# Performance work log

Measured on AMD Instinct MI355X. Metric: run time of the kernel, lower is better.

## Reference

```python
import jax, jax.numpy as jnp
import numpy as np

MODEL_DIM = 1024
HEADS = 16
HEAD_DIM = MODEL_DIM // HEADS
SEQ = 1024


def setup_inputs() -> dict:
    key0 = jax.random.key(0)
    ks = jax.random.split(key0, 10)
    D, H, d, S = MODEL_DIM, HEADS, HEAD_DIM, SEQ
    s = 1.0 / np.sqrt(D)
    return {
        "value": jax.random.normal(ks[0], (S, D), dtype=jnp.float32),
        "key": jax.random.normal(ks[1], (S, D), dtype=jnp.float32),
        "query": jax.random.normal(ks[2], (S, D), dtype=jnp.float32),
        # per-head projection weights, torch Linear layout (out=d, in=D), stacked over heads
        "Wq": jax.random.uniform(ks[3], (H, d, D), jnp.float32, -s, s),
        "Wk": jax.random.uniform(ks[4], (H, d, D), jnp.float32, -s, s),
        "Wv": jax.random.uniform(ks[5], (H, d, D), jnp.float32, -s, s),
        # u, v biases: torch.rand -> uniform [0,1)
        "u": jax.random.uniform(ks[6], (H, d), dtype=jnp.float32),
        "v": jax.random.uniform(ks[7], (H, d), dtype=jnp.float32),
        "Wo": jax.random.uniform(ks[8], (D, D), jnp.float32, -s, s),
        "bo": jax.random.uniform(ks[9], (D,), jnp.float32, -s, s),
    }


def _rel_pos_R(d, Sq, Sk):
    # pos[i, j] = i - j (Transformer-XL style relative offsets)
    pos = (jnp.arange(Sq)[:, None] - jnp.arange(Sk)[None, :]).astype(jnp.float32)
    inv_freq = 10000.0 ** (-2.0 * jnp.arange(d // 2, dtype=jnp.float32) / d)  # (d/2,)
    ang = pos[None, :, :] * inv_freq[:, None, None]  # (d/2, Sq, Sk)
    # interleave: R[2i] = sin(ang_i), R[2i+1] = cos(ang_i)
    R = jnp.stack([jnp.sin(ang), jnp.cos(ang)], axis=1).reshape(d, Sq, Sk)
    return R


def reference(value, key, query, Wq, Wk, Wv, u, v, Wo, bo):
    # defaults of original forward: scale=True, mask=False
    H, d, D = Wq.shape
    Sq, Sk = query.shape[0], key.shape[0]
    q = jnp.einsum("hdD,sD->hsd", Wq, query)   # (H, Sq, d)
    k = jnp.einsum("hdD,tD->htd", Wk, key)     # (H, Sk, d)
    vals = jnp.einsum("hdD,tD->htd", Wv, value)  # (H, Sk, d)

    R = _rel_pos_R(d, Sq, Sk)  # (d, Sq, Sk)

    cc = jnp.einsum("hsd,htd->hst", q, k)       # content-content
    cp = jnp.einsum("hsd,dst->hst", q, R)       # content-position
    uk = jnp.einsum("hd,htd->ht", u, k)[:, None, :]  # global content bias
    vr = jnp.einsum("hd,dst->hst", v, R)        # global position bias

    att = (cc + cp + uk + vr) * (d ** -0.5)
    att = jax.nn.softmax(att, axis=2)

    out = jnp.einsum("hst,htd->hsd", att, vals)  # (H, Sq, d)
    out = out.transpose(1, 0, 2).reshape(Sq, H * d)  # concat heads along feature dim
    return out @ Wo.T + bo
```

## Files before the change

kernel.cpp:

```cpp
#include <hip/hip_runtime.h>
#include <math.h>

#define SQ 1024
#define DIM 1024
#define NH 16
#define HDIM 64

typedef short bf16x8 __attribute__((ext_vector_type(8)));
typedef float f32x4 __attribute__((ext_vector_type(4)));

__device__ __forceinline__ unsigned short f2bf(float x) {
  unsigned int u = __builtin_bit_cast(unsigned int, x);
  u += 0x7FFFu + ((u >> 16) & 1u);
  return (unsigned short)(u >> 16);
}
__device__ __forceinline__ unsigned int pkbf(float a, float b) {
  return (unsigned)f2bf(a) | ((unsigned)f2bf(b) << 16);
}

__global__ __launch_bounds__(256) void prep_kernel(
    const float* __restrict__ query, const float* __restrict__ key_,
    const float* __restrict__ value, const float* __restrict__ Wq,
    const float* __restrict__ Wk, const float* __restrict__ Wv,
    const float* __restrict__ Wo, unsigned short* __restrict__ bfin,
    unsigned short* __restrict__ Rc)
{
  const int b = blockIdx.x;
  if (b < 3584) {
    int gid = b * 256 + threadIdx.x;
    int seg = gid >> 17;
    int off = (gid & 131071) * 8;
    const float* s = seg == 0 ? query : seg == 1 ? key_ : seg == 2 ? value :
                     seg == 3 ? Wq : seg == 4 ? Wk : seg == 5 ? Wv : Wo;
    float4 a = *(const float4*)&s[off];
    float4 c = *(const float4*)&s[off + 4];
    uint4 o;
    o.x = pkbf(a.x, a.y); o.y = pkbf(a.z, a.w);
    o.z = pkbf(c.x, c.y); o.w = pkbf(c.z, c.w);
    *(uint4*)&bfin[(size_t)gid * 8] = o;
  } else {
    int gid = (b - 3584) * 256 + threadIdx.x;
    int p = gid >> 5, f = gid & 31;
    float pos = (float)(p - (SQ - 1));
    float invf = expf(-0.28782313662425575f * (float)f);
    float ang = pos * invf;
    Rc[p * HDIM + 2 * f]     = f2bf(sinf(ang));
    Rc[p * HDIM + 2 * f + 1] = f2bf(cosf(ang));
  }
}

__global__ __launch_bounds__(256) void gemm_qkv(
    const unsigned short* __restrict__ bfin,
    unsigned short* __restrict__ qu, unsigned short* __restrict__ qv,
    unsigned short* __restrict__ kkp, unsigned short* __restrict__ vvpT,
    const float* __restrict__ u, const float* __restrict__ v)
{
  __shared__ short As[2][64 * 72];
  __shared__ short Bs[2][64 * 72];
  const int z = blockIdx.z;
  const unsigned short* A = bfin + (size_t)z * (1 << 20);
  const unsigned short* B = bfin + (size_t)(3 + z) * (1 << 20);
  const int tid = threadIdx.x;
  const int bm = blockIdx.y * 64, bn = blockIdx.x * 64;
  const int w = tid >> 6, l = tid & 63, g = l >> 4, q = l & 15;
  const int wr = w >> 1, wc = w & 1;
  const int srow = tid >> 2, sc = (tid & 3) * 16;
  const unsigned short* Arow = A + (bm + srow) * DIM + sc;
  const unsigned short* Brow = B + (bn + srow) * DIM + sc;
  f32x4 acc[2][2] = {};

  uint4 a0 = *(const uint4*)&Arow[0];
  uint4 a1 = *(const uint4*)&Arow[8];
  uint4 b0 = *(const uint4*)&Brow[0];
  uint4 b1 = *(const uint4*)&Brow[8];
  *(uint4*)&As[0][srow * 72 + sc]     = a0;
  *(uint4*)&As[0][srow * 72 + sc + 8] = a1;
  *(uint4*)&Bs[0][srow * 72 + sc]     = b0;
  *(uint4*)&Bs[0][srow * 72 + sc + 8] = b1;
  __syncthreads();

  #pragma unroll 2
  for (int k0 = 0; k0 < DIM; k0 += 64) {
    const int cur = (k0 >> 6) & 1;
    const bool more = (k0 + 64 < DIM);
    if (more) {
      a0 = *(const uint4*)&Arow[k0 + 64];
      a1 = *(const uint4*)&Arow[k0 + 64 + 8];
      b0 = *(const uint4*)&Brow[k0 + 64];
      b1 = *(const uint4*)&Brow[k0 + 64 + 8];
    }
    #pragma unroll
    for (int ks = 0; ks < 2; ks++) {
      bf16x8 fa0 = *(const bf16x8*)&As[cur][(wr * 32 + q) * 72      + ks * 32 + g * 8];
      bf16x8 fa1 = *(const bf16x8*)&As[cur][(wr * 32 + 16 + q) * 72 + ks * 32 + g * 8];
      bf16x8 fb0 = *(const bf16x8*)&Bs[cur][(wc * 32 + q) * 72      + ks * 32 + g * 8];
      bf16x8 fb1 = *(const bf16x8*)&Bs[cur][(wc * 32 + 16 + q) * 72 + ks * 32 + g * 8];
      acc[0][0] = __builtin_amdgcn_mfma_f32_16x16x32_bf16(fa0, fb0, acc[0][0], 0, 0, 0);
      acc[0][1] = __builtin_amdgcn_mfma_f32_16x16x32_bf16(fa0, fb1, acc[0][1], 0, 0, 0);
      acc[1][0] = __builtin_amdgcn_mfma_f32_16x16x32_bf16(fa1, fb0, acc[1][0], 0, 0, 0);
      acc[1][1] = __builtin_amdgcn_mfma_f32_16x16x32_bf16(fa1, fb1, acc[1][1], 0, 0, 0);
    }
    if (more) {
      *(uint4*)&As[cur ^ 1][srow * 72 + sc]     = a0;
      *(uint4*)&As[cur ^ 1][srow * 72 + sc + 8] = a1;
      *(uint4*)&Bs[cur ^ 1][srow * 72 + sc]     = b0;
      *(uint4*)&Bs[cur ^ 1][srow * 72 + sc + 8] = b1;
      __syncthreads();
    }
  }

  #pragma unroll
  for (int i = 0; i < 2; i++) {
    #pragma unroll
    for (int j = 0; j < 2; j++) {
      const int m0 = bm + wr * 32 + i * 16 + g * 4;
      const int n  = bn + wc * 32 + j * 16 + q;
      if (z == 0) {
        float uu = u[n], vv = v[n];
        #pragma unroll
        for (int r = 0; r < 4; r++) {
          qu[(m0 + r) * DIM + n] = f2bf((acc[i][j][r] + uu) * 0.125f);
          qv[(m0 + r) * DIM + n] = f2bf((acc[i][j][r] + vv) * 0.125f);
        }
      } else if (z == 1) {
        #pragma unroll
        for (int r = 0; r < 4; r++)
          kkp[(m0 + r) * DIM + n] = f2bf(acc[i][j][r]);
      } else {
        ushort4 pk;
        pk.x = f2bf(acc[i][j][0]); pk.y = f2bf(acc[i][j][1]);
        pk.z = f2bf(acc[i][j][2]); pk.w = f2bf(acc[i][j][3]);
        *(ushort4*)&vvpT[n * SQ + m0] = pk;
      }
    }
  }
}

__global__ __launch_bounds__(256) void gemm_out(
    const unsigned short* __restrict__ A, const unsigned short* __restrict__ B,
    float* __restrict__ out, const float* __restrict__ bo)
{
  __shared__ short As[2][64 * 72];
  __shared__ short Bs[2][64 * 72];
  const int tid = threadIdx.x;
  const int bm = blockIdx.y * 64, bn = blockIdx.x * 64;
  const int w = tid >> 6, l = tid & 63, g = l >> 4, q = l & 15;
  const int wr = w >> 1, wc = w & 1;
  const int srow = tid >> 2, sc = (tid & 3) * 16;
  const unsigned short* Arow = A + (bm + srow) * DIM + sc;
  const unsigned short* Brow = B + (bn + srow) * DIM + sc;
  f32x4 acc[2][2] = {};

  uint4 a0 = *(const uint4*)&Arow[0];
  uint4 a1 = *(const uint4*)&Arow[8];
  uint4 b0 = *(const uint4*)&Brow[0];
  uint4 b1 = *(const uint4*)&Brow[8];
  *(uint4*)&As[0][srow * 72 + sc]     = a0;
  *(uint4*)&As[0][srow * 72 + sc + 8] = a1;
  *(uint4*)&Bs[0][srow * 72 + sc]     = b0;
  *(uint4*)&Bs[0][srow * 72 + sc + 8] = b1;
  __syncthreads();

  #pragma unroll 2
  for (int k0 = 0; k0 < DIM; k0 += 64) {
    const int cur = (k0 >> 6) & 1;
    const bool more = (k0 + 64 < DIM);
    if (more) {
      a0 = *(const uint4*)&Arow[k0 + 64];
      a1 = *(const uint4*)&Arow[k0 + 64 + 8];
      b0 = *(const uint4*)&Brow[k0 + 64];
      b1 = *(const uint4*)&Brow[k0 + 64 + 8];
    }
    #pragma unroll
    for (int ks = 0; ks < 2; ks++) {
      bf16x8 fa0 = *(const bf16x8*)&As[cur][(wr * 32 + q) * 72      + ks * 32 + g * 8];
      bf16x8 fa1 = *(const bf16x8*)&As[cur][(wr * 32 + 16 + q) * 72 + ks * 32 + g * 8];
      bf16x8 fb0 = *(const bf16x8*)&Bs[cur][(wc * 32 + q) * 72      + ks * 32 + g * 8];
      bf16x8 fb1 = *(const bf16x8*)&Bs[cur][(wc * 32 + 16 + q) * 72 + ks * 32 + g * 8];
      acc[0][0] = __builtin_amdgcn_mfma_f32_16x16x32_bf16(fa0, fb0, acc[0][0], 0, 0, 0);
      acc[0][1] = __builtin_amdgcn_mfma_f32_16x16x32_bf16(fa0, fb1, acc[0][1], 0, 0, 0);
      acc[1][0] = __builtin_amdgcn_mfma_f32_16x16x32_bf16(fa1, fb0, acc[1][0], 0, 0, 0);
      acc[1][1] = __builtin_amdgcn_mfma_f32_16x16x32_bf16(fa1, fb1, acc[1][1], 0, 0, 0);
    }
    if (more) {
      *(uint4*)&As[cur ^ 1][srow * 72 + sc]     = a0;
      *(uint4*)&As[cur ^ 1][srow * 72 + sc + 8] = a1;
      *(uint4*)&Bs[cur ^ 1][srow * 72 + sc]     = b0;
      *(uint4*)&Bs[cur ^ 1][srow * 72 + sc + 8] = b1;
      __syncthreads();
    }
  }

  #pragma unroll
  for (int i = 0; i < 2; i++) {
    #pragma unroll
    for (int j = 0; j < 2; j++) {
      const int m0 = bm + wr * 32 + i * 16 + g * 4;
      const int n  = bn + wc * 32 + j * 16 + q;
      float bb = bo[n];
      #pragma unroll
      for (int r = 0; r < 4; r++)
        out[(m0 + r) * DIM + n] = acc[i][j][r] + bb;
    }
  }
}

__global__ __launch_bounds__(256) void attn_mfma(
    const unsigned short* __restrict__ qu, const unsigned short* __restrict__ qv,
    const unsigned short* __restrict__ kkp, const unsigned short* __restrict__ vvpT,
    const unsigned short* __restrict__ Rc, float* __restrict__ PO,
    float* __restrict__ ML)
{
  __shared__ short Ks[64 * 72];
  __shared__ short Vs[64 * 72];
  __shared__ short Rcs[128 * 72];
  __shared__ short Ps[64 * 72];
  __shared__ float Gs[64 * 84];

  const int tid = threadIdx.x;
  const int h  = blockIdx.x >> 4;
  const int s0 = (blockIdx.x & 15) * 64;
  const int th = blockIdx.y;
  const int w = tid >> 6, l = tid & 63, g = l >> 4, q = l & 15;
  const int col0 = h * HDIM;

  const int sw = s0 + w * 16 + q;
  bf16x8 qub[2], qvb[2];
  qub[0] = *(const bf16x8*)&qu[sw * DIM + col0 + g * 8];
  qub[1] = *(const bf16x8*)&qu[sw * DIM + col0 + 32 + g * 8];
  qvb[0] = *(const bf16x8*)&qv[sw * DIM + col0 + g * 8];
  qvb[1] = *(const bf16x8*)&qv[sw * DIM + col0 + 32 + g * 8];

  f32x4 accO[4] = {};
  float m_run = -1e30f, l_run = 0.f;

  const int srow = tid >> 2, sc = (tid & 3) * 16;
  const int rrow = tid >> 1, rc = (tid & 1) * 32;

  const int tstart = th * 512, tend = th * 512 + 512;

  uint4 kr0, kr1, vr0, vr1, rr0, rr1, rr2, rr3;
  {
    const int t0 = tstart;
    kr0 = *(const uint4*)&kkp[(t0 + srow) * DIM + col0 + sc];
    kr1 = *(const uint4*)&kkp[(t0 + srow) * DIM + col0 + sc + 8];
    vr0 = *(const uint4*)&vvpT[(col0 + srow) * SQ + t0 + sc];
    vr1 = *(const uint4*)&vvpT[(col0 + srow) * SQ + t0 + sc + 8];
    const int P0 = s0 - t0 + 960;
    rr0 = *(const uint4*)&Rc[(P0 + rrow) * HDIM + rc];
    rr1 = *(const uint4*)&Rc[(P0 + rrow) * HDIM + rc + 8];
    rr2 = *(const uint4*)&Rc[(P0 + rrow) * HDIM + rc + 16];
    rr3 = *(const uint4*)&Rc[(P0 + rrow) * HDIM + rc + 24];
    *(uint4*)&Ks[srow * 72 + sc]      = kr0;
    *(uint4*)&Ks[srow * 72 + sc + 8]  = kr1;
    *(uint4*)&Vs[srow * 72 + sc]      = vr0;
    *(uint4*)&Vs[srow * 72 + sc + 8]  = vr1;
    *(uint4*)&Rcs[rrow * 72 + rc]      = rr0;
    *(uint4*)&Rcs[rrow * 72 + rc + 8]  = rr1;
    *(uint4*)&Rcs[rrow * 72 + rc + 16] = rr2;
    *(uint4*)&Rcs[rrow * 72 + rc + 24] = rr3;
  }
  __syncthreads();

  for (int t0 = tstart; t0 < tend; t0 += 64) {
    const bool more = (t0 + 64 < tend);
    if (more) {
      const int tn = t0 + 64;
      kr0 = *(const uint4*)&kkp[(tn + srow) * DIM + col0 + sc];
      kr1 = *(const uint4*)&kkp[(tn + srow) * DIM + col0 + sc + 8];
      vr0 = *(const uint4*)&vvpT[(col0 + srow) * SQ + tn + sc];
      vr1 = *(const uint4*)&vvpT[(col0 + srow) * SQ + tn + sc + 8];
      const int P0 = s0 - tn + 960;
      rr0 = *(const uint4*)&Rc[(P0 + rrow) * HDIM + rc];
      rr1 = *(const uint4*)&Rc[(P0 + rrow) * HDIM + rc + 8];
      rr2 = *(const uint4*)&Rc[(P0 + rrow) * HDIM + rc + 16];
      rr3 = *(const uint4*)&Rc[(P0 + rrow) * HDIM + rc + 24];
    }

    f32x4 accS[4] = {};
    f32x4 accG[5] = {};
    #pragma unroll
    for (int ks = 0; ks < 2; ks++) {
      #pragma unroll
      for (int tf = 0; tf < 4; tf++) {
        bf16x8 a = *(const bf16x8*)&Ks[(tf * 16 + q) * 72 + ks * 32 + g * 8];
        accS[tf] = __builtin_amdgcn_mfma_f32_16x16x32_bf16(a, qub[ks], accS[tf], 0, 0, 0);
      }
      #pragma unroll
      for (int pf = 0; pf < 5; pf++) {
        bf16x8 a = *(const bf16x8*)&Rcs[(w * 16 + pf * 16 + q) * 72 + ks * 32 + g * 8];
        accG[pf] = __builtin_amdgcn_mfma_f32_16x16x32_bf16(a, qvb[ks], accG[pf], 0, 0, 0);
      }
    }
    #pragma unroll
    for (int pf = 0; pf < 5; pf++)
      *(f32x4*)&Gs[(w * 16 + q) * 84 + pf * 16 + g * 4] = accG[pf];

    float pvals[16];
    float mx = -1e30f;
    #pragma unroll
    for (int tf = 0; tf < 4; tf++) {
      #pragma unroll
      for (int r = 0; r < 4; r++) {
        int t_rel = tf * 16 + g * 4 + r;
        float sval = accS[tf][r] + Gs[(w * 16 + q) * 84 + (q - t_rel + 63)];
        pvals[tf * 4 + r] = sval;
        mx = fmaxf(mx, sval);
      }
    }
    mx = fmaxf(mx, __shfl_xor(mx, 16));
    mx = fmaxf(mx, __shfl_xor(mx, 32));
    float m_new = fmaxf(m_run, mx);
    float scale = __expf(m_run - m_new);
    float rsum = 0.f;
    #pragma unroll
    for (int i = 0; i < 16; i++) {
      float p = __expf(pvals[i] - m_new);
      pvals[i] = p;
      rsum += p;
    }
    rsum += __shfl_xor(rsum, 16);
    rsum += __shfl_xor(rsum, 32);
    l_run = l_run * scale + rsum;
    m_run = m_new;
    #pragma unroll
    for (int df = 0; df < 4; df++) {
      #pragma unroll
      for (int r = 0; r < 4; r++) accO[df][r] *= scale;
    }
    #pragma unroll
    for (int tf = 0; tf < 4; tf++) {
      unsigned int lo = pkbf(pvals[tf * 4 + 0], pvals[tf * 4 + 1]);
      unsigned int hi = pkbf(pvals[tf * 4 + 2], pvals[tf * 4 + 3]);
      *(uint2*)&Ps[(w * 16 + q) * 72 + tf * 16 + g * 4] = make_uint2(lo, hi);
    }
    #pragma unroll
    for (int ks = 0; ks < 2; ks++) {
      bf16x8 b = *(const bf16x8*)&Ps[(w * 16 + q) * 72 + ks * 32 + g * 8];
      #pragma unroll
      for (int df = 0; df < 4; df++) {
        bf16x8 a = *(const bf16x8*)&Vs[(df * 16 + q) * 72 + ks * 32 + g * 8];
        accO[df] = __builtin_amdgcn_mfma_f32_16x16x32_bf16(a, b, accO[df], 0, 0, 0);
      }
    }

    if (more) {
      __syncthreads();
      *(uint4*)&Ks[srow * 72 + sc]      = kr0;
      *(uint4*)&Ks[srow * 72 + sc + 8]  = kr1;
      *(uint4*)&Vs[srow * 72 + sc]      = vr0;
      *(uint4*)&Vs[srow * 72 + sc + 8]  = vr1;
      *(uint4*)&Rcs[rrow * 72 + rc]      = rr0;
      *(uint4*)&Rcs[rrow * 72 + rc + 8]  = rr1;
      *(uint4*)&Rcs[rrow * 72 + rc + 16] = rr2;
      *(uint4*)&Rcs[rrow * 72 + rc + 24] = rr3;
      __syncthreads();
    }
  }

  const int tile = blockIdx.x * 2 + th;
  float* POt = PO + (size_t)tile * 4096;
  const int sl = w * 16 + q;
  #pragma unroll
  for (int df = 0; df < 4; df++)
    *(f32x4*)&POt[sl * 64 + df * 16 + g * 4] = accO[df];
  if (g == 0) {
    ML[tile * 128 + sl * 2]     = m_run;
    ML[tile * 128 + sl * 2 + 1] = l_run;
  }
}

__global__ __launch_bounds__(256) void attn_combine(
    const float* __restrict__ PO, const float* __restrict__ ML,
    unsigned short* __restrict__ attout)
{
  int gid = blockIdx.x * 256 + threadIdx.x;
  int s  = gid >> 8;
  int c  = (gid & 255) * 4;
  int h  = c >> 6;
  int sb = s >> 6, sl = s & 63;
  int tA = (h * 16 + sb) * 2, tB = tA + 1;
  float mA = ML[tA * 128 + sl * 2], lA = ML[tA * 128 + sl * 2 + 1];
  float mB = ML[tB * 128 + sl * 2], lB = ML[tB * 128 + sl * 2 + 1];
  float m = fmaxf(mA, mB);
  float wA = __expf(mA - m), wB = __expf(mB - m);
  float inv = 1.f / (lA * wA + lB * wB);
  wA *= inv; wB *= inv;
  int dl = c & 63;
  float4 a = *(const float4*)&PO[(size_t)tA * 4096 + sl * 64 + dl];
  float4 b = *(const float4*)&PO[(size_t)tB * 4096 + sl * 64 + dl];
  uint2 o;
  o.x = pkbf(a.x * wA + b.x * wB, a.y * wA + b.y * wB);
  o.y = pkbf(a.z * wA + b.z * wB, a.w * wA + b.w * wB);
  *(uint2*)&attout[s * DIM + c] = o;
}

extern "C" void kernel_launch(void* const* d_in, const int* in_sizes, int n_in,
                              void* d_out, int out_size, void* d_ws, size_t ws_size,
                              hipStream_t stream) {
  const float* value = (const float*)d_in[0];
  const float* key   = (const float*)d_in[1];
  const float* query = (const float*)d_in[2];
  const float* Wq    = (const float*)d_in[3];
  const float* Wk    = (const float*)d_in[4];
  const float* Wv    = (const float*)d_in[5];
  const float* u     = (const float*)d_in[6];
  const float* v     = (const float*)d_in[7];
  const float* Wo    = (const float*)d_in[8];
  const float* bo    = (const float*)d_in[9];
  float* out = (float*)d_out;

  unsigned short* ws = (unsigned short*)d_ws;
  unsigned short* bfin   = ws;
  unsigned short* qu_p   = bfin   + 7 * (1 << 20);
  unsigned short* qv_p   = qu_p   + (1 << 20);
  unsigned short* kkp    = qv_p   + (1 << 20);
  unsigned short* vvpT   = kkp    + (1 << 20);
  unsigned short* attout = vvpT   + (1 << 20);
  unsigned short* Rc     = attout + (1 << 20);
  float* PO = (float*)(Rc + 2048 * 64);
  float* ML = PO + (size_t)512 * 4096;

  prep_kernel<<<3840, 256, 0, stream>>>(query, key, value, Wq, Wk, Wv, Wo, bfin, Rc);

  dim3 gqkv(16, 16, 3);
  gemm_qkv<<<gqkv, 256, 0, stream>>>(bfin, qu_p, qv_p, kkp, vvpT, u, v);

  dim3 gattn(NH * (SQ / 64), 2);
  attn_mfma<<<gattn, 256, 0, stream>>>(qu_p, qv_p, kkp, vvpT, Rc, PO, ML);
  attn_combine<<<1024, 256, 0, stream>>>(PO, ML, attout);

  dim3 gg(16, 16);
  gemm_out<<<gg, 256, 0, stream>>>(attout, bfin + 6 * (1 << 20), out, bo);
}
```

Measured before the change: 142.0 us.

## Fuse split-K attention halves into one block and shrink output GEMM tiles

The attention kernel now runs both key halves as two 4-wave groups inside a single 512-thread block and merges their partial outputs through shared memory. This removes the separate combine kernel, one launch, and the global PO/ML round trip. The relative-position tile is no longer staged in shared memory; its MFMA fragments are read directly from global memory, trading LDS staging and barriers for uncached-pattern global loads. The output GEMM uses 32x64 tiles, doubling the block count to improve occupancy, at the cost of half the threads idling on A-tile loads.

```diff
diff --git a/kernel.cpp b/kernel.cpp
--- a/kernel.cpp
+++ b/kernel.cpp
@@ -140,25 +140,30 @@
     const unsigned short* __restrict__ A, const unsigned short* __restrict__ B,
     float* __restrict__ out, const float* __restrict__ bo)
 {
-  __shared__ short As[2][64 * 72];
+  __shared__ short As[2][32 * 72];
   __shared__ short Bs[2][64 * 72];
   const int tid = threadIdx.x;
-  const int bm = blockIdx.y * 64, bn = blockIdx.x * 64;
+  const int bm = blockIdx.y * 32, bn = blockIdx.x * 64;
   const int w = tid >> 6, l = tid & 63, g = l >> 4, q = l & 15;
   const int wr = w >> 1, wc = w & 1;
-  const int srow = tid >> 2, sc = (tid & 3) * 16;
-  const unsigned short* Arow = A + (bm + srow) * DIM + sc;
-  const unsigned short* Brow = B + (bn + srow) * DIM + sc;
-  f32x4 acc[2][2] = {};
-
-  uint4 a0 = *(const uint4*)&Arow[0];
-  uint4 a1 = *(const uint4*)&Arow[8];
-  uint4 b0 = *(const uint4*)&Brow[0];
-  uint4 b1 = *(const uint4*)&Brow[8];
-  *(uint4*)&As[0][srow * 72 + sc]     = a0;
-  *(uint4*)&As[0][srow * 72 + sc + 8] = a1;
-  *(uint4*)&Bs[0][srow * 72 + sc]     = b0;
-  *(uint4*)&Bs[0][srow * 72 + sc + 8] = b1;
+  const int srowB = tid >> 2, scB = (tid & 3) * 16;
+  const int srowA = (tid & 127) >> 2, scA = (tid & 3) * 16;
+  const bool doA = (tid < 128);
+  const unsigned short* ArowP = A + (bm + srowA) * DIM + scA;
+  const unsigned short* BrowP = B + (bn + srowB) * DIM + scB;
+  f32x4 acc[2] = {};
+
+  uint4 a0 = {}, a1 = {};
+  uint4 b0 = *(const uint4*)&BrowP[0];
+  uint4 b1 = *(const uint4*)&BrowP[8];
+  if (doA) {
+    a0 = *(const uint4*)&ArowP[0];
+    a1 = *(const uint4*)&ArowP[8];
+    *(uint4*)&As[0][srowA * 72 + scA]     = a0;
+    *(uint4*)&As[0][srowA * 72 + scA + 8] = a1;
+  }
+  *(uint4*)&Bs[0][srowB * 72 + scB]     = b0;
+  *(uint4*)&Bs[0][srowB * 72 + scB + 8] = b1;
   __syncthreads();
 
   #pragma unroll 2
@@ -166,65 +171,63 @@
     const int cur = (k0 >> 6) & 1;
     const bool more = (k0 + 64 < DIM);
     if (more) {
-      a0 = *(const uint4*)&Arow[k0 + 64];
-      a1 = *(const uint4*)&Arow[k0 + 64 + 8];
-      b0 = *(const uint4*)&Brow[k0 + 64];
-      b1 = *(const uint4*)&Brow[k0 + 64 + 8];
+      if (doA) {
+        a0 = *(const uint4*)&ArowP[k0 + 64];
+        a1 = *(const uint4*)&ArowP[k0 + 64 + 8];
+      }
+      b0 = *(const uint4*)&BrowP[k0 + 64];
+      b1 = *(const uint4*)&BrowP[k0 + 64 + 8];
     }
     #pragma unroll
     for (int ks = 0; ks < 2; ks++) {
-      bf16x8 fa0 = *(const bf16x8*)&As[cur][(wr * 32 + q) * 72      + ks * 32 + g * 8];
-      bf16x8 fa1 = *(const bf16x8*)&As[cur][(wr * 32 + 16 + q) * 72 + ks * 32 + g * 8];
+      bf16x8 fa  = *(const bf16x8*)&As[cur][(wr * 16 + q) * 72      + ks * 32 + g * 8];
       bf16x8 fb0 = *(const bf16x8*)&Bs[cur][(wc * 32 + q) * 72      + ks * 32 + g * 8];
       bf16x8 fb1 = *(const bf16x8*)&Bs[cur][(wc * 32 + 16 + q) * 72 + ks * 32 + g * 8];
-      acc[0][0] = __builtin_amdgcn_mfma_f32_16x16x32_bf16(fa0, fb0, acc[0][0], 0, 0, 0);
-      acc[0][1] = __builtin_amdgcn_mfma_f32_16x16x32_bf16(fa0, fb1, acc[0][1], 0, 0, 0);
-      acc[1][0] = __builtin_amdgcn_mfma_f32_16x16x32_bf16(fa1, fb0, acc[1][0], 0, 0, 0);
-      acc[1][1] = __builtin_amdgcn_mfma_f32_16x16x32_bf16(fa1, fb1, acc[1][1], 0, 0, 0);
-    }
-    if (more) {
-      *(uint4*)&As[cur ^ 1][srow * 72 + sc]     = a0;
-      *(uint4*)&As[cur ^ 1][srow * 72 + sc + 8] = a1;
-      *(uint4*)&Bs[cur ^ 1][srow * 72 + sc]     = b0;
-      *(uint4*)&Bs[cur ^ 1][srow * 72 + sc + 8] = b1;
+      acc[0] = __builtin_amdgcn_mfma_f32_16x16x32_bf16(fa, fb0, acc[0], 0, 0, 0);
+      acc[1] = __builtin_amdgcn_mfma_f32_16x16x32_bf16(fa, fb1, acc[1], 0, 0, 0);
+    }
+    if (more) {
       __syncthreads();
+      if (doA) {
+        *(uint4*)&As[cur ^ 1][srowA * 72 + scA]     = a0;
+        *(uint4*)&As[cur ^ 1][srowA * 72 + scA + 8] = a1;
+      }
+      *(uint4*)&Bs[cur ^ 1][srowB * 72 + scB]     = b0;
+      *(uint4*)&Bs[cur ^ 1][srowB * 72 + scB + 8] = b1;
+      __syncthreads();
     }
   }
 
   #pragma unroll
-  for (int i = 0; i < 2; i++) {
-    #pragma unroll
-    for (int j = 0; j < 2; j++) {
-      const int m0 = bm + wr * 32 + i * 16 + g * 4;
-      const int n  = bn + wc * 32 + j * 16 + q;
-      float bb = bo[n];
-      #pragma unroll
-      for (int r = 0; r < 4; r++)
-        out[(m0 + r) * DIM + n] = acc[i][j][r] + bb;
-    }
-  }
-}
-
-__global__ __launch_bounds__(256) void attn_mfma(
+  for (int j = 0; j < 2; j++) {
+    const int m0 = bm + wr * 16 + g * 4;
+    const int n  = bn + wc * 32 + j * 16 + q;
+    float bb = bo[n];
+    #pragma unroll
+    for (int r = 0; r < 4; r++)
+      out[(m0 + r) * DIM + n] = acc[j][r] + bb;
+  }
+}
+
+__global__ __launch_bounds__(512) void attn_mfma(
     const unsigned short* __restrict__ qu, const unsigned short* __restrict__ qv,
     const unsigned short* __restrict__ kkp, const unsigned short* __restrict__ vvpT,
-    const unsigned short* __restrict__ Rc, float* __restrict__ PO,
-    float* __restrict__ ML)
+    const unsigned short* __restrict__ Rc, unsigned short* __restrict__ attout)
 {
-  __shared__ short Ks[64 * 72];
-  __shared__ short Vs[64 * 72];
-  __shared__ short Rcs[128 * 72];
-  __shared__ short Ps[64 * 72];
-  __shared__ float Gs[64 * 84];
+  __shared__ short Ks[2][64 * 72];
+  __shared__ short Vs[2][64 * 72];
+  __shared__ short Ps[2][64 * 72];
+  __shared__ float Gs[2][64 * 84];
+  __shared__ float2 mlS[2][64];
 
   const int tid = threadIdx.x;
   const int h  = blockIdx.x >> 4;
   const int s0 = (blockIdx.x & 15) * 64;
-  const int th = blockIdx.y;
-  const int w = tid >> 6, l = tid & 63, g = l >> 4, q = l & 15;
+  const int w = tid >> 6, th = w >> 2, ws = w & 3;
+  const int l = tid & 63, g = l >> 4, q = l & 15;
   const int col0 = h * HDIM;
 
-  const int sw = s0 + w * 16 + q;
+  const int sw = s0 + ws * 16 + q;
   bf16x8 qub[2], qvb[2];
   qub[0] = *(const bf16x8*)&qu[sw * DIM + col0 + g * 8];
   qub[1] = *(const bf16x8*)&qu[sw * DIM + col0 + 32 + g * 8];
@@ -234,31 +237,20 @@
   f32x4 accO[4] = {};
   float m_run = -1e30f, l_run = 0.f;
 
-  const int srow = tid >> 2, sc = (tid & 3) * 16;
-  const int rrow = tid >> 1, rc = (tid & 1) * 32;
-
-  const int tstart = th * 512, tend = th * 512 + 512;
-
-  uint4 kr0, kr1, vr0, vr1, rr0, rr1, rr2, rr3;
+  const int tid8 = tid & 255;
+  const int srow = tid8 >> 2, sc = (tid8 & 3) * 16;
+  const int tstart = th * 512, tend = tstart + 512;
+
+  uint4 kr0, kr1, vr0, vr1;
   {
-    const int t0 = tstart;
-    kr0 = *(const uint4*)&kkp[(t0 + srow) * DIM + col0 + sc];
-    kr1 = *(const uint4*)&kkp[(t0 + srow) * DIM + col0 + sc + 8];
-    vr0 = *(const uint4*)&vvpT[(col0 + srow) * SQ + t0 + sc];
-    vr1 = *(const uint4*)&vvpT[(col0 + srow) * SQ + t0 + sc + 8];
-    const int P0 = s0 - t0 + 960;
-    rr0 = *(const uint4*)&Rc[(P0 + rrow) * HDIM + rc];
-    rr1 = *(const uint4*)&Rc[(P0 + rrow) * HDIM + rc + 8];
-    rr2 = *(const uint4*)&Rc[(P0 + rrow) * HDIM + rc + 16];
-    rr3 = *(const uint4*)&Rc[(P0 + rrow) * HDIM + rc + 24];
-    *(uint4*)&Ks[srow * 72 + sc]      = kr0;
-    *(uint4*)&Ks[srow * 72 + sc + 8]  = kr1;
-    *(uint4*)&Vs[srow * 72 + sc]      = vr0;
-    *(uint4*)&Vs[srow * 72 + sc + 8]  = vr1;
-    *(uint4*)&Rcs[rrow * 72 + rc]      = rr0;
-    *(uint4*)&Rcs[rrow * 72 + rc + 8]  = rr1;
-    *(uint4*)&Rcs[rrow * 72 + rc + 16] = rr2;
-    *(uint4*)&Rcs[rrow * 72 + rc + 24] = rr3;
+    kr0 = *(const uint4*)&kkp[(tstart + srow) * DIM + col0 + sc];
+    kr1 = *(const uint4*)&kkp[(tstart + srow) * DIM + col0 + sc + 8];
+    vr0 = *(const uint4*)&vvpT[(col0 + srow) * SQ + tstart + sc];
+    vr1 = *(const uint4*)&vvpT[(col0 + srow) * SQ + tstart + sc + 8];
+    *(uint4*)&Ks[th][srow * 72 + sc]     = kr0;
+    *(uint4*)&Ks[th][srow * 72 + sc + 8] = kr1;
+    *(uint4*)&Vs[th][srow * 72 + sc]     = vr0;
+    *(uint4*)&Vs[th][srow * 72 + sc + 8] = vr1;
   }
   __syncthreads();
 
@@ -270,12 +262,8 @@
       kr1 = *(const uint4*)&kkp[(tn + srow) * DIM + col0 + sc + 8];
       vr0 = *(const uint4*)&vvpT[(col0 + srow) * SQ + tn + sc];
       vr1 = *(const uint4*)&vvpT[(col0 + srow) * SQ + tn + sc + 8];
-      const int P0 = s0 - tn + 960;
-      rr0 = *(const uint4*)&Rc[(P0 + rrow) * HDIM + rc];
-      rr1 = *(const uint4*)&Rc[(P0 + rrow) * HDIM + rc + 8];
-      rr2 = *(const uint4*)&Rc[(P0 + rrow) * HDIM + rc + 16];
-      rr3 = *(const uint4*)&Rc[(P0 + rrow) * HDIM + rc + 24];
-    }
+    }
+    const int P0 = s0 - t0 + 960;
 
     f32x4 accS[4] = {};
     f32x4 accG[5] = {};
@@ -283,18 +271,18 @@
     for (int ks = 0; ks < 2; ks++) {
       #pragma unroll
       for (int tf = 0; tf < 4; tf++) {
-        bf16x8 a = *(const bf16x8*)&Ks[(tf * 16 + q) * 72 + ks * 32 + g * 8];
+        bf16x8 a = *(const bf16x8*)&Ks[th][(tf * 16 + q) * 72 + ks * 32 + g * 8];
         accS[tf] = __builtin_amdgcn_mfma_f32_16x16x32_bf16(a, qub[ks], accS[tf], 0, 0, 0);
       }
       #pragma unroll
       for (int pf = 0; pf < 5; pf++) {
-        bf16x8 a = *(const bf16x8*)&Rcs[(w * 16 + pf * 16 + q) * 72 + ks * 32 + g * 8];
+        bf16x8 a = *(const bf16x8*)&Rc[(size_t)(P0 + ws * 16 + pf * 16 + q) * HDIM + ks * 32 + g * 8];
         accG[pf] = __builtin_amdgcn_mfma_f32_16x16x32_bf16(a, qvb[ks], accG[pf], 0, 0, 0);
       }
     }
     #pragma unroll
     for (int pf = 0; pf < 5; pf++)
-      *(f32x4*)&Gs[(w * 16 + q) * 84 + pf * 16 + g * 4] = accG[pf];
+      *(f32x4*)&Gs[th][(ws * 16 + q) * 84 + pf * 16 + g * 4] = accG[pf];
 
     float pvals[16];
     float mx = -1e30f;
@@ -303,7 +291,7 @@
       #pragma unroll
       for (int r = 0; r < 4; r++) {
         int t_rel = tf * 16 + g * 4 + r;
-        float sval = accS[tf][r] + Gs[(w * 16 + q) * 84 + (q - t_rel + 63)];
+        float sval = accS[tf][r] + Gs[th][(ws * 16 + q) * 84 + (q - t_rel + 63)];
         pvals[tf * 4 + r] = sval;
         mx = fmaxf(mx, sval);
       }
@@ -332,67 +320,58 @@
     for (int tf = 0; tf < 4; tf++) {
       unsigned int lo = pkbf(pvals[tf * 4 + 0], pvals[tf * 4 + 1]);
       unsigned int hi = pkbf(pvals[tf * 4 + 2], pvals[tf * 4 + 3]);
-      *(uint2*)&Ps[(w * 16 + q) * 72 + tf * 16 + g * 4] = make_uint2(lo, hi);
+      *(uint2*)&Ps[th][(ws * 16 + q) * 72 + tf * 16 + g * 4] = make_uint2(lo, hi);
     }
     #pragma unroll
     for (int ks = 0; ks < 2; ks++) {
-      bf16x8 b = *(const bf16x8*)&Ps[(w * 16 + q) * 72 + ks * 32 + g * 8];
+      bf16x8 b = *(const bf16x8*)&Ps[th][(ws * 16 + q) * 72 + ks * 32 + g * 8];
       #pragma unroll
       for (int df = 0; df < 4; df++) {
-        bf16x8 a = *(const bf16x8*)&Vs[(df * 16 + q) * 72 + ks * 32 + g * 8];
+        bf16x8 a = *(const bf16x8*)&Vs[th][(df * 16 + q) * 72 + ks * 32 + g * 8];
         accO[df] = __builtin_amdgcn_mfma_f32_16x16x32_bf16(a, b, accO[df], 0, 0, 0);
       }
     }
 
     if (more) {
       __syncthreads();
-      *(uint4*)&Ks[srow * 72 + sc]      = kr0;
-      *(uint4*)&Ks[srow * 72 + sc + 8]  = kr1;
-      *(uint4*)&Vs[srow * 72 + sc]      = vr0;
-      *(uint4*)&Vs[srow * 72 + sc + 8]  = vr1;
-      *(uint4*)&Rcs[rrow * 72 + rc]      = rr0;
-      *(uint4*)&Rcs[rrow * 72 + rc + 8]  = rr1;
-      *(uint4*)&Rcs[rrow * 72 + rc + 16] = rr2;
-      *(uint4*)&Rcs[rrow * 72 + rc + 24] = rr3;
+      *(uint4*)&Ks[th][srow * 72 + sc]     = kr0;
+      *(uint4*)&Ks[th][srow * 72 + sc + 8] = kr1;
+      *(uint4*)&Vs[th][srow * 72 + sc]     = vr0;
+      *(uint4*)&Vs[th][srow * 72 + sc + 8] = vr1;
       __syncthreads();
     }
   }
 
-  const int tile = blockIdx.x * 2 + th;
-  float* POt = PO + (size_t)tile * 4096;
-  const int sl = w * 16 + q;
-  #pragma unroll
-  for (int df = 0; df < 4; df++)
-    *(f32x4*)&POt[sl * 64 + df * 16 + g * 4] = accO[df];
-  if (g == 0) {
-    ML[tile * 128 + sl * 2]     = m_run;
-    ML[tile * 128 + sl * 2 + 1] = l_run;
-  }
-}
-
-__global__ __launch_bounds__(256) void attn_combine(
-    const float* __restrict__ PO, const float* __restrict__ ML,
-    unsigned short* __restrict__ attout)
-{
-  int gid = blockIdx.x * 256 + threadIdx.x;
-  int s  = gid >> 8;
-  int c  = (gid & 255) * 4;
-  int h  = c >> 6;
-  int sb = s >> 6, sl = s & 63;
-  int tA = (h * 16 + sb) * 2, tB = tA + 1;
-  float mA = ML[tA * 128 + sl * 2], lA = ML[tA * 128 + sl * 2 + 1];
-  float mB = ML[tB * 128 + sl * 2], lB = ML[tB * 128 + sl * 2 + 1];
-  float m = fmaxf(mA, mB);
-  float wA = __expf(mA - m), wB = __expf(mB - m);
-  float inv = 1.f / (lA * wA + lB * wB);
-  wA *= inv; wB *= inv;
-  int dl = c & 63;
-  float4 a = *(const float4*)&PO[(size_t)tA * 4096 + sl * 64 + dl];
-  float4 b = *(const float4*)&PO[(size_t)tB * 4096 + sl * 64 + dl];
-  uint2 o;
-  o.x = pkbf(a.x * wA + b.x * wB, a.y * wA + b.y * wB);
-  o.y = pkbf(a.z * wA + b.z * wB, a.w * wA + b.w * wB);
-  *(uint2*)&attout[s * DIM + c] = o;
+  {
+    float* Os = (float*)&Gs[th][0];
+    const int sl = ws * 16 + q;
+    #pragma unroll
+    for (int df = 0; df < 4; df++)
+      *(f32x4*)&Os[sl * 84 + df * 16 + g * 4] = accO[df];
+    if (g == 0) mlS[th][sl] = make_float2(m_run, l_run);
+  }
+  __syncthreads();
+
+  {
+    const int s = tid >> 3, d0 = (tid & 7) * 8;
+    float2 Am = mlS[0][s], Bm = mlS[1][s];
+    float m = fmaxf(Am.x, Bm.x);
+    float wA = __expf(Am.x - m), wB = __expf(Bm.x - m);
+    float inv = 1.f / (Am.y * wA + Bm.y * wB);
+    wA *= inv; wB *= inv;
+    const float* OsA = (const float*)&Gs[0][0];
+    const float* OsB = (const float*)&Gs[1][0];
+    float4 a0 = *(const float4*)&OsA[s * 84 + d0];
+    float4 a1 = *(const float4*)&OsA[s * 84 + d0 + 4];
+    float4 b0 = *(const float4*)&OsB[s * 84 + d0];
+    float4 b1 = *(const float4*)&OsB[s * 84 + d0 + 4];
+    uint4 o;
+    o.x = pkbf(a0.x * wA + b0.x * wB, a0.y * wA + b0.y * wB);
+    o.y = pkbf(a0.z * wA + b0.z * wB, a0.w * wA + b0.w * wB);
+    o.z = pkbf(a1.x * wA + b1.x * wB, a1.y * wA + b1.y * wB);
+    o.w = pkbf(a1.z * wA + b1.z * wB, a1.w * wA + b1.w * wB);
+    *(uint4*)&attout[(s0 + s) * DIM + col0 + d0] = o;
+  }
 }
 
 extern "C" void kernel_launch(void* const* d_in, const int* in_sizes, int n_in,
@@ -418,18 +397,14 @@
   unsigned short* vvpT   = kkp    + (1 << 20);
   unsigned short* attout = vvpT   + (1 << 20);
   unsigned short* Rc     = attout + (1 << 20);
-  float* PO = (float*)(Rc + 2048 * 64);
-  float* ML = PO + (size_t)512 * 4096;
 
   prep_kernel<<<3840, 256, 0, stream>>>(query, key, value, Wq, Wk, Wv, Wo, bfin, Rc);
 
   dim3 gqkv(16, 16, 3);
   gemm_qkv<<<gqkv, 256, 0, stream>>>(bfin, qu_p, qv_p, kkp, vvpT, u, v);
 
-  dim3 gattn(NH * (SQ / 64), 2);
-  attn_mfma<<<gattn, 256, 0, stream>>>(qu_p, qv_p, kkp, vvpT, Rc, PO, ML);
-  attn_combine<<<1024, 256, 0, stream>>>(PO, ML, attout);
-
-  dim3 gg(16, 16);
-  gemm_out<<<gg, 256, 0, stream>>>(attout, bfin + 6 * (1 << 20), out, bo);
-}
+  attn_mfma<<<NH * (SQ / 64), 512, 0, stream>>>(qu_p, qv_p, kkp, vvpT, Rc, attout);
+
+  dim3 ggo(16, 32);
+  gemm_out<<<ggo, 256, 0, stream>>>(attout, bfin + 6 * (1 << 20), out, bo);
+}
```

New measurement: 148.8 us. 1.05x slower.
